# Performance work log

Measured on AMD Instinct MI355X. Metric: run time of the kernel, lower is better.

The kernel has to match this reference:

```python
import jax, jax.numpy as jnp
import numpy as np

N_NODES = 100_000
N_EDGES = 1_600_000
F_NODE = 4
F_EDGE = 5
H = 64
EDGE_DIM = 2 * H + F_EDGE  # 133


def setup_inputs() -> dict:
    key = jax.random.key(0)
    ks = jax.random.split(key, 24)
    s = 0.05
    inp = {
        "node_feat": jax.random.normal(ks[0], (N_NODES, F_NODE), jnp.float32),
        "edge_feat": jax.random.normal(ks[1], (N_EDGES, F_EDGE), jnp.float32),
        "src": jax.random.randint(ks[2], (N_EDGES,), 0, N_NODES, jnp.int32),
        "dst": jax.random.randint(ks[3], (N_EDGES,), 0, N_NODES, jnp.int32),
        # SAGEConv 1 (DGL mean aggregator: fc_self(h) + fc_neigh(mean_neigh(h)) + bias)
        "W1s": jax.random.normal(ks[4], (F_NODE, H), jnp.float32) * s,
        "W1n": jax.random.normal(ks[5], (F_NODE, H), jnp.float32) * s,
        "b1": jnp.zeros((H,), jnp.float32),
        # SAGEConv 2
        "W2s": jax.random.normal(ks[6], (H, H), jnp.float32) * s,
        "W2n": jax.random.normal(ks[7], (H, H), jnp.float32) * s,
        "b2": jnp.zeros((H,), jnp.float32),
        # nodeprocess: Linear(F_NODE? no -> applied to h which is H-dim) Linear(H? )
        # NOTE: original declares nn.Linear(num_node_features, hidden) but applies it to h (H-dim);
        # we follow the applied shape, Linear(H, H), so the math is runnable and consistent.
        "Wnp": jax.random.normal(ks[8], (H, H), jnp.float32) * s,
        "bnp": jnp.zeros((H,), jnp.float32),
        # edgeprocess: Linear(EDGE_DIM, H) -> tanh -> Linear(H, 1)
        "We1": jax.random.normal(ks[9], (EDGE_DIM, H), jnp.float32) * s,
        "be1": jnp.zeros((H,), jnp.float32),
        "We2": jax.random.normal(ks[10], (H, 1), jnp.float32) * s,
        "be2": jnp.zeros((1,), jnp.float32),
        # lin1: Linear(EDGE_DIM, H); lin2: Linear(H, 1)
        "Wl1": jax.random.normal(ks[11], (EDGE_DIM, H), jnp.float32) * s,
        "bl1": jnp.zeros((H,), jnp.float32),
        "Wl2": jax.random.normal(ks[12], (H, 1), jnp.float32) * s,
        "bl2": jnp.zeros((1,), jnp.float32),
    }
    return inp


def _sage_mean(h, src, dst, Ws, Wn, b, inv_deg):
    # project first (cheaper: N x d instead of E x d), then gather+scatter-mean
    msg = (h @ Wn)[src]                                    # [E, H]
    agg = jax.ops.segment_sum(msg, dst, num_segments=h.shape[0]) * inv_deg
    return h @ Ws + agg + b


def reference(node_feat, edge_feat, src, dst,
              W1s, W1n, b1, W2s, W2n, b2,
              Wnp, bnp, We1, be1, We2, be2,
              Wl1, bl1, Wl2, bl2):
    n = node_feat.shape[0]
    deg = jax.ops.segment_sum(jnp.ones_like(dst, jnp.float32), dst, num_segments=n)
    inv_deg = (1.0 / jnp.maximum(deg, 1.0))[:, None]       # [N,1]

    h = jax.nn.relu(_sage_mean(node_feat, src, dst, W1s, W1n, b1, inv_deg))
    h = jax.nn.relu(_sage_mean(h, src, dst, W2s, W2n, b2, inv_deg))

    h_src = jax.nn.relu(h[src] @ Wnp + bnp)                # [E, H]
    h_dst = jax.nn.relu(h[dst] @ Wnp + bnp)                # [E, H]
    ef = jnp.concatenate([h_src, h_dst, edge_feat], axis=1)  # [E, 133]

    w = jax.nn.sigmoid(jnp.tanh(ef @ We1 + be1) @ We2 + be2)  # [E, 1]
    efw = ef * w
    out = jax.nn.relu(efw @ Wl1 + bl1)                     # dropout: eval mode (identity)
    return out @ Wl2 + bl2                                 # [E, 1]
```

## Files before the change

### kernel.cpp

```cpp
#include <hip/hip_runtime.h>
#include <math.h>


__device__ __forceinline__ float fast_tanh(float x) {
    x = fminf(fmaxf(x, -15.f), 15.f);
    float e2 = __expf(2.f * x);
    return (e2 - 1.f) * __builtin_amdgcn_rcpf(e2 + 1.f);
}
__device__ __forceinline__ float fast_sigmoid(float x) {
    x = fminf(fmaxf(x, -60.f), 60.f);
    return __builtin_amdgcn_rcpf(1.f + __expf(-x));
}
__device__ __forceinline__ unsigned short f2bf(float f) {
    unsigned u = __float_as_uint(f);
    u = u + 0x7FFFu + ((u >> 16) & 1u);
    return (unsigned short)(u >> 16);
}
__device__ __forceinline__ float bflo(unsigned u) { return __uint_as_float(u << 16); }
__device__ __forceinline__ float bfhi(unsigned u) { return __uint_as_float(u & 0xFFFF0000u); }

__device__ __forceinline__ float dpp_sum16(float x) {
    int t;
    t = __builtin_amdgcn_update_dpp(0, __float_as_int(x), 0xB1, 0xF, 0xF, true);
    x += __int_as_float(t);
    t = __builtin_amdgcn_update_dpp(0, __float_as_int(x), 0x4E, 0xF, 0xF, true);
    x += __int_as_float(t);
    t = __builtin_amdgcn_update_dpp(0, __float_as_int(x), 0x141, 0xF, 0xF, true);
    x += __int_as_float(t);
    t = __builtin_amdgcn_update_dpp(0, __float_as_int(x), 0x140, 0xF, 0xF, true);
    x += __int_as_float(t);
    return x;
}

__global__ void rank_k(const int* __restrict__ dst, int* __restrict__ deg,
                       int* __restrict__ rank, int E) {
    int e = blockIdx.x * blockDim.x + threadIdx.x;
    if (e < E) rank[e] = atomicAdd(&deg[dst[e]], 1);
}

__global__ void scan1_k(const int* __restrict__ deg, int* __restrict__ off,
                        int* __restrict__ bsum, int N) {
    __shared__ int tmp[256];
    int i = blockIdx.x * 256 + threadIdx.x;
    int v = (i < N) ? deg[i] : 0;
    tmp[threadIdx.x] = v;
    __syncthreads();
#pragma unroll
    for (int s = 1; s < 256; s <<= 1) {
        int t = (threadIdx.x >= s) ? tmp[threadIdx.x - s] : 0;
        __syncthreads();
        tmp[threadIdx.x] += t;
        __syncthreads();
    }
    if (i < N) off[i] = tmp[threadIdx.x] - v;
    if (threadIdx.x == 255) bsum[blockIdx.x] = tmp[255];
}

__global__ void scan2_k(int* __restrict__ bsum, int nb) {
    __shared__ int tmp[512];
    int i = threadIdx.x;
    int v = (i < nb) ? bsum[i] : 0;
    tmp[i] = v;
    __syncthreads();
#pragma unroll
    for (int s = 1; s < 512; s <<= 1) {
        int t = (i >= s) ? tmp[i - s] : 0;
        __syncthreads();
        tmp[i] += t;
        __syncthreads();
    }
    if (i < nb) bsum[i] = tmp[i] - v;
}

__global__ void scan3_k(int* __restrict__ off, const int* __restrict__ bsum,
                        int N, int E) {
    int i = blockIdx.x * 256 + threadIdx.x;
    if (i < N) off[i] += bsum[blockIdx.x];
    if (i == 0) off[N] = E;
}

__global__ void fill2_k(const int* __restrict__ src, const int* __restrict__ dst,
                        const int* __restrict__ off, const int* __restrict__ rank,
                        int2* __restrict__ csr, int E) {
    int e = blockIdx.x * blockDim.x + threadIdx.x;
    if (e >= E) return;
    csr[off[dst[e]] + rank[e]] = make_int2(src[e], e);
}

__global__ __launch_bounds__(256, 8)
void aggh1f_k(const int* __restrict__ off, const int2* __restrict__ csr,
              const float* __restrict__ nf,
              const float* __restrict__ W1s, const float* __restrict__ W1n,
              const float* __restrict__ b1, unsigned short* __restrict__ h1s, int N) {
    int n = blockIdx.x * 4 + (threadIdx.x >> 6);
    if (n >= N) return;
    int l = threadIdx.x & 63;
    int s0 = off[n], s1 = off[n + 1];
    float4 a = {0.f, 0.f, 0.f, 0.f};
    for (int i = s0 + l; i < s1; i += 64) {
        float4 r = ((const float4*)nf)[csr[i].x];
        a.x += r.x; a.y += r.y; a.z += r.z; a.w += r.w;
    }
#pragma unroll
    for (int m = 1; m < 64; m <<= 1) {
        a.x += __shfl_xor(a.x, m);
        a.y += __shfl_xor(a.y, m);
        a.z += __shfl_xor(a.z, m);
        a.w += __shfl_xor(a.w, m);
    }
    float invd = 1.f / fmaxf((float)(s1 - s0), 1.f);
    a.x *= invd; a.y *= invd; a.z *= invd; a.w *= invd;
    float4 r = ((const float4*)nf)[n];
    float v = b1[l]
            + r.x * W1s[l] + r.y * W1s[64 + l] + r.z * W1s[128 + l] + r.w * W1s[192 + l]
            + a.x * W1n[l] + a.y * W1n[64 + l] + a.z * W1n[128 + l] + a.w * W1n[192 + l];
    h1s[(size_t)n * 64 + l] = f2bf(fmaxf(v, 0.f));
}

__global__ __launch_bounds__(256, 8)
void gatherh1_k(const int* __restrict__ off, const int2* __restrict__ csr,
                const unsigned* __restrict__ h1b, float* __restrict__ aggh1, int N) {
    int n = blockIdx.x * 4 + (threadIdx.x >> 6);
    if (n >= N) return;
    int l = threadIdx.x & 63;
    int g = l >> 4, q = l & 15;
    int s0 = off[n], s1 = off[n + 1];
    float4 acc = {0.f, 0.f, 0.f, 0.f};
    int i = s0;
    for (; i + 8 <= s1; i += 8) {
        int r0 = csr[i + g].x;
        int r1 = csr[i + 4 + g].x;
        uint2 v0 = *(const uint2*)&h1b[(size_t)r0 * 32 + q * 2];
        uint2 v1 = *(const uint2*)&h1b[(size_t)r1 * 32 + q * 2];
        acc.x += bflo(v0.x) + bflo(v1.x);
        acc.y += bfhi(v0.x) + bfhi(v1.x);
        acc.z += bflo(v0.y) + bflo(v1.y);
        acc.w += bfhi(v0.y) + bfhi(v1.y);
    }
    for (; i + 4 <= s1; i += 4) {
        int r0 = csr[i + g].x;
        uint2 v0 = *(const uint2*)&h1b[(size_t)r0 * 32 + q * 2];
        acc.x += bflo(v0.x); acc.y += bfhi(v0.x);
        acc.z += bflo(v0.y); acc.w += bfhi(v0.y);
    }
    int rem = s1 - i;
    if (g < rem) {
        int r0 = csr[i + g].x;
        uint2 v0 = *(const uint2*)&h1b[(size_t)r0 * 32 + q * 2];
        acc.x += bflo(v0.x); acc.y += bfhi(v0.x);
        acc.z += bflo(v0.y); acc.w += bfhi(v0.y);
    }
#pragma unroll
    for (int m = 16; m <= 32; m <<= 1) {
        acc.x += __shfl_xor(acc.x, m);
        acc.y += __shfl_xor(acc.y, m);
        acc.z += __shfl_xor(acc.z, m);
        acc.w += __shfl_xor(acc.w, m);
    }
    if (l < 16) {
        float invd = 1.f / fmaxf((float)(s1 - s0), 1.f);
        acc.x *= invd; acc.y *= invd; acc.z *= invd; acc.w *= invd;
        *(float4*)&aggh1[(size_t)n * 64 + q * 4] = acc;
    }
}

__device__ __forceinline__ void mac64(const float (*hT)[68], const float (*wt)[64],
                                      int rr, int cr, float acc[4][4]) {
#pragma unroll 8
    for (int k = 0; k < 64; ++k) {
        float4 a = *(const float4*)&hT[k][rr];
        float4 w = *(const float4*)&wt[k][cr];
        acc[0][0] = fmaf(a.x, w.x, acc[0][0]); acc[0][1] = fmaf(a.x, w.y, acc[0][1]);
        acc[0][2] = fmaf(a.x, w.z, acc[0][2]); acc[0][3] = fmaf(a.x, w.w, acc[0][3]);
        acc[1][0] = fmaf(a.y, w.x, acc[1][0]); acc[1][1] = fmaf(a.y, w.y, acc[1][1]);
        acc[1][2] = fmaf(a.y, w.z, acc[1][2]); acc[1][3] = fmaf(a.y, w.w, acc[1][3]);
        acc[2][0] = fmaf(a.z, w.x, acc[2][0]); acc[2][1] = fmaf(a.z, w.y, acc[2][1]);
        acc[2][2] = fmaf(a.z, w.z, acc[2][2]); acc[2][3] = fmaf(a.z, w.w, acc[2][3]);
        acc[3][0] = fmaf(a.w, w.x, acc[3][0]); acc[3][1] = fmaf(a.w, w.y, acc[3][1]);
        acc[3][2] = fmaf(a.w, w.z, acc[3][2]); acc[3][3] = fmaf(a.w, w.w, acc[3][3]);
    }
}

__global__ __launch_bounds__(256, 4)
void node_mlp_k(const unsigned* __restrict__ h1b, const float* __restrict__ aggh1,
                const float* __restrict__ W2s, const float* __restrict__ W2n,
                const float* __restrict__ b2, const float* __restrict__ Wnp,
                const float* __restrict__ bnp, const float* __restrict__ We1,
                const float* __restrict__ Wl1, unsigned short* __restrict__ ST, int N) {
    __shared__ __align__(16) float hT[64][68];
    __shared__ __align__(16) float wt[64][64];
    const int t = threadIdx.x;
    const int m0 = blockIdx.x * 64;
    const int cr = (t & 15) << 2, rr = (t >> 4) << 2;
    float acc[4][4] = {};

#pragma unroll
    for (int it = 0; it < 8; ++it) {
        int u = it * 256 + t;
        int m = u >> 5, p = u & 31;
        int row = m0 + m;
        unsigned v = (row < N) ? h1b[(size_t)row * 32 + p] : 0u;
        hT[2 * p][m] = bflo(v);
        hT[2 * p + 1][m] = bfhi(v);
    }
#pragma unroll
    for (int it = 0; it < 16; ++it) {
        int k = it * 4 + (t >> 6), c = t & 63;
        wt[k][c] = W2s[k * 64 + c];
    }
    __syncthreads();
    mac64(hT, wt, rr, cr, acc);
    __syncthreads();

#pragma unroll
    for (int it = 0; it < 16; ++it) {
        int m = it * 4 + (t >> 6), k = t & 63, row = m0 + m;
        hT[k][m] = (row < N) ? aggh1[(size_t)row * 64 + k] : 0.f;
    }
#pragma unroll
    for (int it = 0; it < 16; ++it) {
        int k = it * 4 + (t >> 6), c = t & 63;
        wt[k][c] = W2n[k * 64 + c];
    }
    __syncthreads();
    mac64(hT, wt, rr, cr, acc);
    __syncthreads();

#pragma unroll
    for (int i = 0; i < 4; ++i)
#pragma unroll
        for (int q = 0; q < 4; ++q)
            hT[cr + q][rr + i] = fmaxf(acc[i][q] + b2[cr + q], 0.f);
#pragma unroll
    for (int it = 0; it < 16; ++it) {
        int k = it * 4 + (t >> 6), c = t & 63;
        wt[k][c] = Wnp[k * 64 + c];
    }
    __syncthreads();
    float ac2[4][4] = {};
    mac64(hT, wt, rr, cr, ac2);
    __syncthreads();

#pragma unroll
    for (int i = 0; i < 4; ++i)
#pragma unroll
        for (int q = 0; q < 4; ++q)
            hT[cr + q][rr + i] = fmaxf(ac2[i][q] + bnp[cr + q], 0.f);
    __syncthreads();

    for (int cb = 0; cb < 4; ++cb) {
        if (cb) __syncthreads();
#pragma unroll
        for (int it = 0; it < 16; ++it) {
            int k = it * 4 + (t >> 6), c = t & 63;
            int cglob = cb * 64 + c;
            int half = cglob >> 7, cc = cglob & 127;
            int jj = cc >> 1, p = cc & 1;
            const float* W = p ? Wl1 : We1;
            wt[k][c] = W[(half * 64 + k) * 64 + jj];
        }
        __syncthreads();
        float ac3[4][4] = {};
        mac64(hT, wt, rr, cr, ac3);
#pragma unroll
        for (int i = 0; i < 4; ++i) {
            int row = m0 + rr + i;
            if (row >= N) continue;
            ushort4 pk;
            pk.x = f2bf(ac3[i][0]); pk.y = f2bf(ac3[i][1]);
            pk.z = f2bf(ac3[i][2]); pk.w = f2bf(ac3[i][3]);
            *(ushort4*)&ST[(size_t)row * 256 + cb * 64 + cr] = pk;
        }
    }
}

__global__ void edge_k(const int* __restrict__ off, const int2* __restrict__ csr,
                       const float* __restrict__ ef, const unsigned* __restrict__ ST32,
                       const float* __restrict__ We1, const float* __restrict__ be1,
                       const float* __restrict__ We2, const float* __restrict__ be2,
                       const float* __restrict__ Wl1, const float* __restrict__ bl1,
                       const float* __restrict__ Wl2, const float* __restrict__ bl2,
                       float* __restrict__ out, int N) {
    int n = blockIdx.x * 4 + (threadIdx.x >> 6);
    if (n >= N) return;
    const int l = threadIdx.x & 63;
    const int g = l >> 4;
    const int q = l & 15;
    const int j0 = q << 2;
    int s0 = off[n], s1 = off[n + 1];
    if (s0 >= s1) return;

    float4 wet[5], wlt[5];
#pragma unroll
    for (int k = 0; k < 5; ++k) {
        wet[k] = *(const float4*)&We1[(128 + k) * 64 + j0];
        wlt[k] = *(const float4*)&Wl1[(128 + k) * 64 + j0];
    }
    const float4 vbe1 = *(const float4*)&be1[j0];
    const float4 vwe2 = *(const float4*)&We2[j0];
    const float4 vbl1 = *(const float4*)&bl1[j0];
    const float4 vwl2 = *(const float4*)&Wl2[j0];
    const float vbe2 = be2[0], vbl2 = bl2[0];

    uint4 pw = *(const uint4*)&ST32[(size_t)n * 128 + 64 + j0];
    const float4 tb = {bflo(pw.x) + vbe1.x, bflo(pw.y) + vbe1.y,
                       bflo(pw.z) + vbe1.z, bflo(pw.w) + vbe1.w};
    const float4 ub = {bfhi(pw.x), bfhi(pw.y), bfhi(pw.z), bfhi(pw.w)};

    const bool gb1 = (g & 1), gb2 = (g & 2);

    for (int i = s0; i < s1; i += 4) {
        int ii = i + g;
        bool act = ii < s1;
        int2 se = csr[act ? ii : s0];
        uint4 sw = *(const uint4*)&ST32[(size_t)se.x * 128 + j0];
        float4 t4 = {bflo(sw.x) + tb.x, bflo(sw.y) + tb.y,
                     bflo(sw.z) + tb.z, bflo(sw.w) + tb.w};
        float4 u4 = {bfhi(sw.x) + ub.x, bfhi(sw.y) + ub.y,
                     bfhi(sw.z) + ub.z, bfhi(sw.w) + ub.w};
        int e0 = __builtin_amdgcn_readlane(se.y, 0);
        int e1 = __builtin_amdgcn_readlane(se.y, 16);
        int e2 = __builtin_amdgcn_readlane(se.y, 32);
        int e3 = __builtin_amdgcn_readlane(se.y, 48);
        const float* p0 = ef + (size_t)e0 * 5;
        const float* p1 = ef + (size_t)e1 * 5;
        const float* p2 = ef + (size_t)e2 * 5;
        const float* p3 = ef + (size_t)e3 * 5;
#pragma unroll
        for (int k = 0; k < 5; ++k) {
            float a01 = gb1 ? p1[k] : p0[k];
            float a23 = gb1 ? p3[k] : p2[k];
            float ek  = gb2 ? a23 : a01;
            t4.x = fmaf(ek, wet[k].x, t4.x); t4.y = fmaf(ek, wet[k].y, t4.y);
            t4.z = fmaf(ek, wet[k].z, t4.z); t4.w = fmaf(ek, wet[k].w, t4.w);
            u4.x = fmaf(ek, wlt[k].x, u4.x); u4.y = fmaf(ek, wlt[k].y, u4.y);
            u4.z = fmaf(ek, wlt[k].z, u4.z); u4.w = fmaf(ek, wlt[k].w, u4.w);
        }
        float z = fast_tanh(t4.x) * vwe2.x + fast_tanh(t4.y) * vwe2.y
                + fast_tanh(t4.z) * vwe2.z + fast_tanh(t4.w) * vwe2.w;
        z = dpp_sum16(z);
        float w = fast_sigmoid(z + vbe2);
        float o = fmaxf(fmaf(w, u4.x, vbl1.x), 0.f) * vwl2.x
                + fmaxf(fmaf(w, u4.y, vbl1.y), 0.f) * vwl2.y
                + fmaxf(fmaf(w, u4.z, vbl1.z), 0.f) * vwl2.z
                + fmaxf(fmaf(w, u4.w, vbl1.w), 0.f) * vwl2.w;
        o = dpp_sum16(o);
        if (q == 0 && act) out[se.y] = o + vbl2;
    }
}

extern "C" void kernel_launch(void* const* d_in, const int* in_sizes, int n_in,
                              void* d_out, int out_size, void* d_ws, size_t ws_size,
                              hipStream_t stream) {
    const float* nf  = (const float*)d_in[0];
    const float* ef  = (const float*)d_in[1];
    const int*   src = (const int*)d_in[2];
    const int*   dst = (const int*)d_in[3];
    const float* W1s = (const float*)d_in[4];
    const float* W1n = (const float*)d_in[5];
    const float* b1  = (const float*)d_in[6];
    const float* W2s = (const float*)d_in[7];
    const float* W2n = (const float*)d_in[8];
    const float* b2  = (const float*)d_in[9];
    const float* Wnp = (const float*)d_in[10];
    const float* bnp = (const float*)d_in[11];
    const float* We1 = (const float*)d_in[12];
    const float* be1 = (const float*)d_in[13];
    const float* We2 = (const float*)d_in[14];
    const float* be2 = (const float*)d_in[15];
    const float* Wl1 = (const float*)d_in[16];
    const float* bl1 = (const float*)d_in[17];
    const float* Wl2 = (const float*)d_in[18];
    const float* bl2 = (const float*)d_in[19];

    const int N = in_sizes[0] / 4;
    const int E = in_sizes[2];

    float* wsf = (float*)d_ws;
    unsigned short* ST = (unsigned short*)wsf;
    float* aggh1 = wsf + (size_t)128 * N;
    unsigned* h1b = (unsigned*)(wsf + (size_t)192 * N);
    int2* csr  = (int2*)(wsf + (size_t)224 * N);
    int*  rank = (int*)(wsf + (size_t)256 * N);
    int*  deg  = (int*)(wsf + (size_t)272 * N);
    int*  off  = deg + N;
    int*  bsum = off + N + 1;
    float* out = (float*)d_out;

    const int nblkN1 = (N + 255) / 256;
    const int nblkE  = (E + 255) / 256;
    const int nblkNw = (N + 3) / 4;
    const int gemmx  = (N + 63) / 64;

    hipMemsetAsync(deg, 0, (size_t)N * sizeof(int), stream);
    rank_k<<<nblkE, 256, 0, stream>>>(dst, deg, rank, E);
    scan1_k<<<nblkN1, 256, 0, stream>>>(deg, off, bsum, N);
    scan2_k<<<1, 512, 0, stream>>>(bsum, nblkN1);
    scan3_k<<<nblkN1, 256, 0, stream>>>(off, bsum, N, E);
    fill2_k<<<nblkE, 256, 0, stream>>>(src, dst, off, rank, csr, E);

    aggh1f_k<<<nblkNw, 256, 0, stream>>>(off, csr, nf, W1s, W1n, b1,
                                         (unsigned short*)h1b, N);

    gatherh1_k<<<nblkNw, 256, 0, stream>>>(off, csr, h1b, aggh1, N);

    node_mlp_k<<<gemmx, 256, 0, stream>>>(h1b, aggh1, W2s, W2n, b2,
                                          Wnp, bnp, We1, Wl1, ST, N);

    edge_k<<<nblkNw, 256, 0, stream>>>(off, csr, ef, (const unsigned*)ST,
                                       We1, be1, We2, be2, Wl1, bl1, Wl2, bl2,
                                       out, N);
}
```

Baseline: 548.5 us.

## Store neighbor mean in bf16, unroll gather, shrink blocks, simplify edge-feature loads

The aggregated h1 neighbor mean is now written as packed bf16 instead of fp32, which halves the write in gatherh1_k and the read in node_mlp_k. The gather loop is unrolled to 16 edges per iteration so more loads are in flight. gatherh1_k and edge_k now run with 128-thread blocks of two nodes each, which gives finer load balance over skewed degrees. In edge_k each lane loads its own edge features directly instead of doing readlane broadcasts and selects, at the cost of redundant per-lane loads and some extra bf16 rounding error in the aggregate.

```diff
diff --git a/kernel.cpp b/kernel.cpp
--- a/kernel.cpp
+++ b/kernel.cpp
@@ -15,6 +15,9 @@
     unsigned u = __float_as_uint(f);
     u = u + 0x7FFFu + ((u >> 16) & 1u);
     return (unsigned short)(u >> 16);
+}
+__device__ __forceinline__ unsigned pack2bf(float lo, float hi) {
+    return ((unsigned)f2bf(hi) << 16) | (unsigned)f2bf(lo);
 }
 __device__ __forceinline__ float bflo(unsigned u) { return __uint_as_float(u << 16); }
 __device__ __forceinline__ float bfhi(unsigned u) { return __uint_as_float(u & 0xFFFF0000u); }
@@ -117,25 +120,29 @@
     h1s[(size_t)n * 64 + l] = f2bf(fmaxf(v, 0.f));
 }
 
-__global__ __launch_bounds__(256, 8)
+__global__ __launch_bounds__(128, 8)
 void gatherh1_k(const int* __restrict__ off, const int2* __restrict__ csr,
-                const unsigned* __restrict__ h1b, float* __restrict__ aggh1, int N) {
-    int n = blockIdx.x * 4 + (threadIdx.x >> 6);
+                const unsigned* __restrict__ h1b, unsigned* __restrict__ ah1b, int N) {
+    int n = blockIdx.x * 2 + (threadIdx.x >> 6);
     if (n >= N) return;
     int l = threadIdx.x & 63;
     int g = l >> 4, q = l & 15;
     int s0 = off[n], s1 = off[n + 1];
     float4 acc = {0.f, 0.f, 0.f, 0.f};
     int i = s0;
-    for (; i + 8 <= s1; i += 8) {
+    for (; i + 16 <= s1; i += 16) {
         int r0 = csr[i + g].x;
         int r1 = csr[i + 4 + g].x;
+        int r2 = csr[i + 8 + g].x;
+        int r3 = csr[i + 12 + g].x;
         uint2 v0 = *(const uint2*)&h1b[(size_t)r0 * 32 + q * 2];
         uint2 v1 = *(const uint2*)&h1b[(size_t)r1 * 32 + q * 2];
-        acc.x += bflo(v0.x) + bflo(v1.x);
-        acc.y += bfhi(v0.x) + bfhi(v1.x);
-        acc.z += bflo(v0.y) + bflo(v1.y);
-        acc.w += bfhi(v0.y) + bfhi(v1.y);
+        uint2 v2 = *(const uint2*)&h1b[(size_t)r2 * 32 + q * 2];
+        uint2 v3 = *(const uint2*)&h1b[(size_t)r3 * 32 + q * 2];
+        acc.x += (bflo(v0.x) + bflo(v1.x)) + (bflo(v2.x) + bflo(v3.x));
+        acc.y += (bfhi(v0.x) + bfhi(v1.x)) + (bfhi(v2.x) + bfhi(v3.x));
+        acc.z += (bflo(v0.y) + bflo(v1.y)) + (bflo(v2.y) + bflo(v3.y));
+        acc.w += (bfhi(v0.y) + bfhi(v1.y)) + (bfhi(v2.y) + bfhi(v3.y));
     }
     for (; i + 4 <= s1; i += 4) {
         int r0 = csr[i + g].x;
@@ -159,8 +166,10 @@
     }
     if (l < 16) {
         float invd = 1.f / fmaxf((float)(s1 - s0), 1.f);
-        acc.x *= invd; acc.y *= invd; acc.z *= invd; acc.w *= invd;
-        *(float4*)&aggh1[(size_t)n * 64 + q * 4] = acc;
+        uint2 pk;
+        pk.x = pack2bf(acc.x * invd, acc.y * invd);
+        pk.y = pack2bf(acc.z * invd, acc.w * invd);
+        *(uint2*)&ah1b[(size_t)n * 32 + q * 2] = pk;
     }
 }
 
@@ -182,7 +191,7 @@
 }
 
 __global__ __launch_bounds__(256, 4)
-void node_mlp_k(const unsigned* __restrict__ h1b, const float* __restrict__ aggh1,
+void node_mlp_k(const unsigned* __restrict__ h1b, const unsigned* __restrict__ ah1b,
                 const float* __restrict__ W2s, const float* __restrict__ W2n,
                 const float* __restrict__ b2, const float* __restrict__ Wnp,
                 const float* __restrict__ bnp, const float* __restrict__ We1,
@@ -213,9 +222,13 @@
     __syncthreads();
 
 #pragma unroll
-    for (int it = 0; it < 16; ++it) {
-        int m = it * 4 + (t >> 6), k = t & 63, row = m0 + m;
-        hT[k][m] = (row < N) ? aggh1[(size_t)row * 64 + k] : 0.f;
+    for (int it = 0; it < 8; ++it) {
+        int u = it * 256 + t;
+        int m = u >> 5, p = u & 31;
+        int row = m0 + m;
+        unsigned v = (row < N) ? ah1b[(size_t)row * 32 + p] : 0u;
+        hT[2 * p][m] = bflo(v);
+        hT[2 * p + 1][m] = bfhi(v);
     }
 #pragma unroll
     for (int it = 0; it < 16; ++it) {
@@ -274,14 +287,15 @@
     }
 }
 
-__global__ void edge_k(const int* __restrict__ off, const int2* __restrict__ csr,
-                       const float* __restrict__ ef, const unsigned* __restrict__ ST32,
-                       const float* __restrict__ We1, const float* __restrict__ be1,
-                       const float* __restrict__ We2, const float* __restrict__ be2,
-                       const float* __restrict__ Wl1, const float* __restrict__ bl1,
-                       const float* __restrict__ Wl2, const float* __restrict__ bl2,
-                       float* __restrict__ out, int N) {
-    int n = blockIdx.x * 4 + (threadIdx.x >> 6);
+__global__ __launch_bounds__(128, 8)
+void edge_k(const int* __restrict__ off, const int2* __restrict__ csr,
+            const float* __restrict__ ef, const unsigned* __restrict__ ST32,
+            const float* __restrict__ We1, const float* __restrict__ be1,
+            const float* __restrict__ We2, const float* __restrict__ be2,
+            const float* __restrict__ Wl1, const float* __restrict__ bl1,
+            const float* __restrict__ Wl2, const float* __restrict__ bl2,
+            float* __restrict__ out, int N) {
+    int n = blockIdx.x * 2 + (threadIdx.x >> 6);
     if (n >= N) return;
     const int l = threadIdx.x & 63;
     const int g = l >> 4;
@@ -307,30 +321,21 @@
                        bflo(pw.z) + vbe1.z, bflo(pw.w) + vbe1.w};
     const float4 ub = {bfhi(pw.x), bfhi(pw.y), bfhi(pw.z), bfhi(pw.w)};
 
-    const bool gb1 = (g & 1), gb2 = (g & 2);
-
     for (int i = s0; i < s1; i += 4) {
         int ii = i + g;
         bool act = ii < s1;
         int2 se = csr[act ? ii : s0];
         uint4 sw = *(const uint4*)&ST32[(size_t)se.x * 128 + j0];
+        const float* ep = ef + (size_t)se.y * 5;
+        float ek0 = ep[0], ek1 = ep[1], ek2 = ep[2], ek3 = ep[3], ek4 = ep[4];
         float4 t4 = {bflo(sw.x) + tb.x, bflo(sw.y) + tb.y,
                      bflo(sw.z) + tb.z, bflo(sw.w) + tb.w};
         float4 u4 = {bfhi(sw.x) + ub.x, bfhi(sw.y) + ub.y,
                      bfhi(sw.z) + ub.z, bfhi(sw.w) + ub.w};
-        int e0 = __builtin_amdgcn_readlane(se.y, 0);
-        int e1 = __builtin_amdgcn_readlane(se.y, 16);
-        int e2 = __builtin_amdgcn_readlane(se.y, 32);
-        int e3 = __builtin_amdgcn_readlane(se.y, 48);
-        const float* p0 = ef + (size_t)e0 * 5;
-        const float* p1 = ef + (size_t)e1 * 5;
-        const float* p2 = ef + (size_t)e2 * 5;
-        const float* p3 = ef + (size_t)e3 * 5;
+        float ekk[5] = {ek0, ek1, ek2, ek3, ek4};
 #pragma unroll
         for (int k = 0; k < 5; ++k) {
-            float a01 = gb1 ? p1[k] : p0[k];
-            float a23 = gb1 ? p3[k] : p2[k];
-            float ek  = gb2 ? a23 : a01;
+            float ek = ekk[k];
             t4.x = fmaf(ek, wet[k].x, t4.x); t4.y = fmaf(ek, wet[k].y, t4.y);
             t4.z = fmaf(ek, wet[k].z, t4.z); t4.w = fmaf(ek, wet[k].w, t4.w);
             u4.x = fmaf(ek, wlt[k].x, u4.x); u4.y = fmaf(ek, wlt[k].y, u4.y);
@@ -378,8 +383,8 @@
 
     float* wsf = (float*)d_ws;
     unsigned short* ST = (unsigned short*)wsf;
-    float* aggh1 = wsf + (size_t)128 * N;
-    unsigned* h1b = (unsigned*)(wsf + (size_t)192 * N);
+    unsigned* ah1b = (unsigned*)(wsf + (size_t)128 * N);
+    unsigned* h1b  = (unsigned*)(wsf + (size_t)192 * N);
     int2* csr  = (int2*)(wsf + (size_t)224 * N);
     int*  rank = (int*)(wsf + (size_t)256 * N);
     int*  deg  = (int*)(wsf + (size_t)272 * N);
@@ -389,7 +394,8 @@
 
     const int nblkN1 = (N + 255) / 256;
     const int nblkE  = (E + 255) / 256;
-    const int nblkNw = (N + 3) / 4;
+    const int nblkNw4 = (N + 3) / 4;
+    const int nblkNw2 = (N + 1) / 2;
     const int gemmx  = (N + 63) / 64;
 
     hipMemsetAsync(deg, 0, (size_t)N * sizeof(int), stream);
@@ -399,15 +405,15 @@
     scan3_k<<<nblkN1, 256, 0, stream>>>(off, bsum, N, E);
     fill2_k<<<nblkE, 256, 0, stream>>>(src, dst, off, rank, csr, E);
 
-    aggh1f_k<<<nblkNw, 256, 0, stream>>>(off, csr, nf, W1s, W1n, b1,
-                                         (unsigned short*)h1b, N);
-
-    gatherh1_k<<<nblkNw, 256, 0, stream>>>(off, csr, h1b, aggh1, N);
-
-    node_mlp_k<<<gemmx, 256, 0, stream>>>(h1b, aggh1, W2s, W2n, b2,
+    aggh1f_k<<<nblkNw4, 256, 0, stream>>>(off, csr, nf, W1s, W1n, b1,
+                                          (unsigned short*)h1b, N);
+
+    gatherh1_k<<<nblkNw2, 128, 0, stream>>>(off, csr, h1b, ah1b, N);
+
+    node_mlp_k<<<gemmx, 256, 0, stream>>>(h1b, ah1b, W2s, W2n, b2,
                                           Wnp, bnp, We1, Wl1, ST, N);
 
-    edge_k<<<nblkNw, 256, 0, stream>>>(off, csr, ef, (const unsigned*)ST,
-                                       We1, be1, We2, be2, Wl1, bl1, Wl2, bl2,
-                                       out, N);
-}
+    edge_k<<<nblkNw2, 128, 0, stream>>>(off, csr, ef, (const unsigned*)ST,
+                                        We1, be1, We2, be2, Wl1, bl1, Wl2, bl2,
+                                        out, N);
+}
```

After: 877.6 us. 1.6x slower.
